# Performance work log

Hardware: AMD Instinct MI355X
Metric: run time of the kernel (lower is better)

Reference implementation:

```python
import jax, jax.numpy as jnp
import numpy as np
from jax import lax

U, K, POOL, STRIDE, FC = 300, 19, 7, 7, 100   # num_units, filter size, maxpool, fc_size
B, L, D = 256, 1000, 4                        # batch, seq len, DNA dim
P = (L - (K - 1) - (POOL - 1) - 1) // STRIDE + 1  # post_pool_size = 140
EPS = 1e-5  # BatchNorm eps (eval mode with running stats; Dropout is identity in eval)


def setup_inputs() -> dict:
    key = jax.random.key(0)
    ks = jax.random.split(key, 24)
    rn = lambda k, shp, s=0.1: jax.random.normal(k, shp, jnp.float32) * s
    return {
        "input_seq": jax.random.normal(ks[0], (B, L, D), jnp.float32),
        # per-unit conv (groups=U on tiled input == plain Conv1d(4, U, K))
        "w_conv": rn(ks[1], (U, D, K)), "b_conv": rn(ks[2], (U,)),
        "g1": 1.0 + rn(ks[3], (U,)), "be1": rn(ks[4], (U,)),
        "m1": rn(ks[5], (U,)), "v1": 1.0 + jax.random.uniform(ks[6], (U,), jnp.float32),
        # per-unit FC1 (grouped 1x1 conv: P -> FC per unit)
        "w_fc1": rn(ks[7], (U, FC, P)), "b_fc1": rn(ks[8], (U, FC)),
        "g2": 1.0 + rn(ks[9], (U, FC)), "be2": rn(ks[10], (U, FC)),
        "m2": rn(ks[11], (U, FC)), "v2": 1.0 + jax.random.uniform(ks[12], (U, FC), jnp.float32),
        # per-unit FC2 (grouped 1x1 conv: FC -> 1 per unit)
        "w_fc2": rn(ks[13], (U, FC)), "b_fc2": rn(ks[14], (U,)),
        "g3": 1.0 + rn(ks[15], (U,)), "be3": rn(ks[16], (U,)),
        "m3": rn(ks[17], (U,)), "v3": 1.0 + jax.random.uniform(ks[18], (U,), jnp.float32),
        # final Linear(U, 1)
        "w_out": rn(ks[19], (U, 1)), "b_out": rn(ks[20], (1,)),
    }


def reference(input_seq, w_conv, b_conv, g1, be1, m1, v1, w_fc1, b_fc1,
              g2, be2, m2, v2, w_fc2, b_fc2, g3, be3, m3, v3, w_out, b_out):
    x = jnp.transpose(input_seq, (0, 2, 1))  # B,D,L
    # grouped conv on input tiled U times: every group sees the same D=4 channels,
    # so it is exactly a plain Conv1d(D, U, K).
    conv = lax.conv_general_dilated(
        x, w_conv, (1,), 'VALID', dimension_numbers=('NCH', 'OIH', 'NCH')
    ) + b_conv[None, :, None]                 # B,U,L' (L'=L-K+1)
    a = (conv - m1[None, :, None]) * (g1 / jnp.sqrt(v1 + EPS))[None, :, None] + be1[None, :, None]
    a = jnp.exp(a)
    pooled = lax.reduce_window(a, -jnp.inf, lax.max,
                               (1, 1, POOL), (1, 1, STRIDE), 'VALID')  # B,U,P
    # Flatten->Unsqueeze->grouped 1x1 conv == per-unit matmul over P
    h = jnp.einsum('bup,ufp->buf', pooled, w_fc1) + b_fc1               # B,U,FC
    h = jax.nn.relu((h - m2) * (g2 / jnp.sqrt(v2 + EPS)) + be2)
    z = jnp.einsum('buf,uf->bu', h, w_fc2) + b_fc2                      # B,U
    z = jax.nn.relu((z - m3) * (g3 / jnp.sqrt(v3 + EPS)) + be3)
    return jax.nn.sigmoid(z @ w_out + b_out)                            # B,1
```

## Files before the change

kernel.cpp:

```cpp
#include <hip/hip_runtime.h>
#include <hip/hip_bf16.h>
#include <math.h>

#define U_   300
#define K_   19
#define FC_  100
#define B_   256
#define L_   1000
#define P_   140
#define EPS_ 1e-5f
#define WLD_ 144

typedef unsigned short ushort_t;
typedef __attribute__((ext_vector_type(8)))  short short8v;
typedef __attribute__((ext_vector_type(16))) float f32x16;

__device__ __forceinline__ ushort_t f2bf(float f) {
    union { float f; unsigned u; } a; a.f = f;
    unsigned r = a.u + 0x7fffu + ((a.u >> 16) & 1u);
    return (ushort_t)(r >> 16);
}

__global__ __launch_bounds__(256, 4)
void pack_conv_k(const float* __restrict__ w_conv, const float* __restrict__ b_conv,
                 const float* __restrict__ g1, const float* __restrict__ be1,
                 const float* __restrict__ m1, const float* __restrict__ v1,
                 ushort_t* __restrict__ w_bf, float* __restrict__ o1g)
{
    const int t = blockIdx.x * 256 + threadIdx.x;
    if (t < 320 * 80) {
        const int u = t / 80, j = t - u * 80;
        float val = 0.f;
        if (u < U_ && j < 76) {
            const int tp = j >> 2;
            const int d  = j & 3;
            const float s1 = g1[u] / sqrtf(v1[u] + EPS_);
            val = w_conv[u * 76 + 19 * d + tp] * s1;
        }
        const int nt = u >> 5, r = u & 31;
        const int kc = j >> 4, rem = j & 15;
        w_bf[nt * 2560 + kc * 512 + r * 16 + rem] = f2bf(val);
    }
    if (t < 320) {
        float o = 0.f;
        if (t < U_) {
            const float s1 = g1[t] / sqrtf(v1[t] + EPS_);
            o = (b_conv[t] - m1[t]) * s1 + be1[t];
        }
        o1g[t] = o;
    }
}

__global__ __launch_bounds__(896, 7)
void conv_mfma_k(const float4* __restrict__ x4,
                 const ushort_t* __restrict__ w_bf,
                 const float* __restrict__ o1g,
                 ushort_t* __restrict__ pooled)
{
    __shared__ ushort_t xls[880];
    const int tid = threadIdx.x;
    const int b   = blockIdx.y;
    const int bx  = blockIdx.x;
    const int w0  = bx * 28;
    const int l0  = w0 * 7;

    if (tid < 220) {
        const int gi = l0 + tid;
        float4 v = make_float4(0.f, 0.f, 0.f, 0.f);
        if (gi < L_) v = x4[(size_t)b * L_ + gi];
        ushort4 pk;
        pk.x = f2bf(v.x); pk.y = f2bf(v.y); pk.z = f2bf(v.z); pk.w = f2bf(v.w);
        *(ushort4*)&xls[4 * tid] = pk;
    }
    __syncthreads();

    const int lane = tid & 63;
    const int wv   = tid >> 6;
    const int mt   = (wv < 7) ? wv : wv - 7;
    const int nth  = (wv < 7) ? 0 : 1;
    const int half = lane >> 5;
    const int r32  = lane & 31;

    const int sreg = (r32 & 3) + 4 * (r32 >> 3);
    const int sh   = (r32 >> 2) & 1;
    const int off  = sreg < 7  ? sreg + 7 * sh
                   : sreg < 14 ? sreg + 7 + 7 * sh
                               : 28 + (sreg - 14) + 2 * sh;

    const char* xb = (const char*)xls + 8 * (28 * mt + off) + 16 * half;
    const char* wbase = (const char*)w_bf + 32 * r32 + 16 * half;

    short8v aA[5];
#pragma unroll
    for (int kc = 0; kc < 5; ++kc)
        aA[kc] = *(const short8v*)(xb + 32 * kc);

    const int pA = w0 + 4 * mt;
    const int nt0 = nth * 5;

    short8v bfr[5];
#pragma unroll
    for (int kc = 0; kc < 5; ++kc)
        bfr[kc] = *(const short8v*)(wbase + nt0 * 5120 + 1024 * kc);
    float o1u = o1g[nt0 * 32 + r32];

    for (int i = 0; i < 5; ++i) {
        const int nt  = nt0 + i;
        const int ntn = (i < 4) ? nt + 1 : nt;
        short8v bnx[5];
        const char* wn = wbase + ntn * 5120;
#pragma unroll
        for (int kc = 0; kc < 5; ++kc)
            bnx[kc] = *(const short8v*)(wn + 1024 * kc);
        const float o1n = o1g[ntn * 32 + r32];

        f32x16 acc = {};
#pragma unroll
        for (int kc = 0; kc < 5; ++kc)
            acc = __builtin_amdgcn_mfma_f32_32x32x16_bf16(aA[kc], bfr[kc], acc, 0, 0, 0);

        float m0 = acc[0], m1 = acc[7];
#pragma unroll
        for (int j = 1; j < 7; ++j)  m0 = fmaxf(m0, acc[j]);
#pragma unroll
        for (int j = 8; j < 14; ++j) m1 = fmaxf(m1, acc[j]);
        const unsigned pk = (unsigned)f2bf(__expf(m0 + o1u)) |
                            ((unsigned)f2bf(__expf(m1 + o1u)) << 16);
        const unsigned ot = __shfl_xor(pk, 32);

        const int u = nt * 32 + r32;
        if (u < U_ && half == 0) {
            ushort4 st;
            st.x = (ushort_t)(pk & 0xffff);
            st.y = (ushort_t)(ot & 0xffff);
            st.z = (ushort_t)(pk >> 16);
            st.w = (ushort_t)(ot >> 16);
            *(ushort4*)&pooled[((size_t)u * B_ + b) * P_ + pA] = st;
        }

#pragma unroll
        for (int kc = 0; kc < 5; ++kc) bfr[kc] = bnx[kc];
        o1u = o1n;
    }
}

__global__ __launch_bounds__(256, 3)
void fc_mfma_k(const ushort_t* __restrict__ pooled,
               const float* __restrict__ w_fc1,
               const float* __restrict__ b_fc1,
               const float* __restrict__ g2,
               const float* __restrict__ be2,
               const float* __restrict__ m2,
               const float* __restrict__ v2,
               const float* __restrict__ w_fc2,
               const float* __restrict__ b_fc2,
               const float* __restrict__ g3,
               const float* __restrict__ be3,
               const float* __restrict__ m3,
               const float* __restrict__ v3,
               float* __restrict__ zT)
{
    __shared__ ushort_t wlds[FC_ * WLD_];
    __shared__ float zred[128][33];
    const int tid  = threadIdx.x;
    const int u    = blockIdx.y;
    const int bt   = blockIdx.x;

    const float* __restrict__ wsrc = w_fc1 + (size_t)u * FC_ * P_;
    for (int idx = tid; idx < FC_ * 35; idx += 256) {
        const int f = idx / 35, j = idx - f * 35;
        const float4 v = *(const float4*)(wsrc + f * P_ + 4 * j);
        ushort4 pk;
        pk.x = f2bf(v.x); pk.y = f2bf(v.y); pk.z = f2bf(v.z); pk.w = f2bf(v.w);
        *(ushort4*)&wlds[f * WLD_ + 4 * j] = pk;
    }
    for (int idx = tid; idx < FC_ * 4; idx += 256) {
        const int f = idx >> 2, k = 140 + (idx & 3);
        wlds[f * WLD_ + k] = 0;
    }
    __syncthreads();

    const int lane = tid & 63;
    const int wv   = tid >> 6;
    const int half = lane >> 5;
    const int r32  = lane & 31;

    const int brow = bt * 128 + wv * 32 + r32;
    const ushort_t* __restrict__ abase =
        pooled + ((size_t)u * B_ + brow) * P_ + half * 8;

    const ushort_t* __restrict__ bl0 = &wlds[r32 * WLD_ + half * 8];
    const ushort_t* __restrict__ bl1 = &wlds[(32 + r32) * WLD_ + half * 8];
    const ushort_t* __restrict__ bl2 = &wlds[(64 + r32) * WLD_ + half * 8];
    const int f3c = (96 + r32 < FC_) ? (96 + r32) : (FC_ - 1);
    const ushort_t* __restrict__ bl3 = &wlds[f3c * WLD_ + half * 8];

    short8v ac = *(const short8v*)(abase);
    f32x16 acc0 = {}, acc1 = {}, acc2 = {}, acc3 = {};
#pragma unroll
    for (int kc = 0; kc < 9; ++kc) {
        const int kn = (kc < 8) ? kc + 1 : kc;
        const short8v an = *(const short8v*)(abase + kn * 16);
        const short8v b0 = *(const short8v*)(bl0 + kc * 16);
        const short8v b1 = *(const short8v*)(bl1 + kc * 16);
        const short8v b2 = *(const short8v*)(bl2 + kc * 16);
        const short8v b3 = *(const short8v*)(bl3 + kc * 16);
        acc0 = __builtin_amdgcn_mfma_f32_32x32x16_bf16(ac, b0, acc0, 0, 0, 0);
        acc1 = __builtin_amdgcn_mfma_f32_32x32x16_bf16(ac, b1, acc1, 0, 0, 0);
        acc2 = __builtin_amdgcn_mfma_f32_32x32x16_bf16(ac, b2, acc2, 0, 0, 0);
        acc3 = __builtin_amdgcn_mfma_f32_32x32x16_bf16(ac, b3, acc3, 0, 0, 0);
        ac = an;
    }

    float s2[4], o2[4], w2[4];
#pragma unroll
    for (int n = 0; n < 4; ++n) {
        const int f = n * 32 + r32;
        if (f < FC_) {
            const int fg = u * FC_ + f;
            const float ss = g2[fg] / sqrtf(v2[fg] + EPS_);
            s2[n] = ss;
            o2[n] = (b_fc1[fg] - m2[fg]) * ss + be2[fg];
            w2[n] = w_fc2[fg];
        } else {
            s2[n] = 0.f; o2[n] = 0.f; w2[n] = 0.f;
        }
    }
#pragma unroll
    for (int rg = 0; rg < 16; ++rg) {
        const int row = (rg & 3) + 8 * (rg >> 2) + 4 * half;
        float s = fmaxf(fmaf(acc0[rg], s2[0], o2[0]), 0.f) * w2[0];
        s = fmaf(fmaxf(fmaf(acc1[rg], s2[1], o2[1]), 0.f), w2[1], s);
        s = fmaf(fmaxf(fmaf(acc2[rg], s2[2], o2[2]), 0.f), w2[2], s);
        s = fmaf(fmaxf(fmaf(acc3[rg], s2[3], o2[3]), 0.f), w2[3], s);
        zred[wv * 32 + row][r32] = s;
    }
    __syncthreads();

    if (tid < 128) {
        float s = 0.f;
#pragma unroll
        for (int j = 0; j < 32; ++j) s += zred[tid][j];
        const float s3 = g3[u] / sqrtf(v3[u] + EPS_);
        const float o3 = (b_fc2[u] - m3[u]) * s3 + be3[u];
        zT[(size_t)(bt * 128 + tid) * 304 + u] = fmaxf(fmaf(s, s3, o3), 0.f);
    }
}

__global__ __launch_bounds__(64, 8)
void out_k(const float* __restrict__ zT,
           const float* __restrict__ w_out,
           const float* __restrict__ b_out,
           float* __restrict__ out)
{
    const int lane = threadIdx.x;
    const int b    = blockIdx.x;
    const float4* zr = (const float4*)(zT + (size_t)b * 304);
    const float4* w4 = (const float4*)w_out;

    float s = 0.f;
    for (int i = lane; i < 75; i += 64) {
        const float4 z = zr[i], w = w4[i];
        s += z.x * w.x + z.y * w.y + z.z * w.z + z.w * w.w;
    }
#pragma unroll
    for (int o = 32; o > 0; o >>= 1) s += __shfl_xor(s, o);
    if (lane == 0)
        out[b] = 1.0f / (1.0f + __expf(-(s + b_out[0])));
}

extern "C" void kernel_launch(void* const* d_in, const int* in_sizes, int n_in,
                              void* d_out, int out_size, void* d_ws, size_t ws_size,
                              hipStream_t stream)
{
    const float* input_seq = (const float*)d_in[0];
    const float* w_conv    = (const float*)d_in[1];
    const float* b_conv    = (const float*)d_in[2];
    const float* g1        = (const float*)d_in[3];
    const float* be1       = (const float*)d_in[4];
    const float* m1        = (const float*)d_in[5];
    const float* v1        = (const float*)d_in[6];
    const float* w_fc1     = (const float*)d_in[7];
    const float* b_fc1     = (const float*)d_in[8];
    const float* g2        = (const float*)d_in[9];
    const float* be2       = (const float*)d_in[10];
    const float* m2        = (const float*)d_in[11];
    const float* v2        = (const float*)d_in[12];
    const float* w_fc2     = (const float*)d_in[13];
    const float* b_fc2     = (const float*)d_in[14];
    const float* g3        = (const float*)d_in[15];
    const float* be3       = (const float*)d_in[16];
    const float* m3        = (const float*)d_in[17];
    const float* v3        = (const float*)d_in[18];
    const float* w_out     = (const float*)d_in[19];
    const float* b_out     = (const float*)d_in[20];

    char* p = (char*)d_ws;
    ushort_t* pooled = (ushort_t*)p;   p += (size_t)B_ * U_ * P_ * 2;
    ushort_t* w_bf   = (ushort_t*)p;   p += 320 * 80 * 2;
    float*    o1g    = (float*)p;      p += 320 * 4;
    float*    zT     = (float*)p;      p += (size_t)B_ * 304 * 4;

    pack_conv_k<<<dim3(100), 256, 0, stream>>>(
        w_conv, b_conv, g1, be1, m1, v1, w_bf, o1g);

    conv_mfma_k<<<dim3(5, B_), 896, 0, stream>>>(
        (const float4*)input_seq, w_bf, o1g, pooled);

    fc_mfma_k<<<dim3(2, U_), 256, 0, stream>>>(
        pooled, w_fc1, b_fc1, g2, be2, m2, v2, w_fc2, b_fc2,
        g3, be3, m3, v3, zT);

    out_k<<<dim3(B_), 64, 0, stream>>>(zT, w_out, b_out, (float*)d_out);
}
```

Measured before the change: 63.06 us.

## Process two batch rows per conv block and remap block ids for XCD locality

Each conv block now handles two batch samples with 7 waves, and every wave covers all 10 unit tiles. Each loaded weight fragment therefore feeds two MFMA chains, halving weight reloads per output and doubling independent MFMA work per wave. The software prefetch of the next weight tile is dropped. Both conv and FC grids become 1D with a swizzled block-id mapping, likely to group related blocks on the same XCD/L2 (the modulo-8 pattern suggests this) and improve cache reuse.

```diff
diff --git a/kernel.cpp b/kernel.cpp
--- a/kernel.cpp
+++ b/kernel.cpp
@@ -51,33 +51,36 @@
     }
 }
 
-__global__ __launch_bounds__(896, 7)
+__global__ __launch_bounds__(448, 4)
 void conv_mfma_k(const float4* __restrict__ x4,
                  const ushort_t* __restrict__ w_bf,
                  const float* __restrict__ o1g,
                  ushort_t* __restrict__ pooled)
 {
-    __shared__ ushort_t xls[880];
+    __shared__ ushort_t xls[2][880];
     const int tid = threadIdx.x;
-    const int b   = blockIdx.y;
-    const int bx  = blockIdx.x;
-    const int w0  = bx * 28;
-    const int l0  = w0 * 7;
-
-    if (tid < 220) {
-        const int gi = l0 + tid;
+    const int bid = blockIdx.x;
+    const int r8 = bid & 7, kk = bid >> 3;
+    const int bx = kk % 5, p8 = kk / 5;
+    const int pair = p8 * 8 + r8;
+    const int b0 = 2 * pair;
+    const int w0 = bx * 28;
+    const int l0 = w0 * 7;
+
+    if (tid < 440) {
+        const int which = (tid >= 220) ? 1 : 0;
+        const int i = tid - 220 * which;
+        const int gi = l0 + i;
         float4 v = make_float4(0.f, 0.f, 0.f, 0.f);
-        if (gi < L_) v = x4[(size_t)b * L_ + gi];
-        ushort4 pk;
-        pk.x = f2bf(v.x); pk.y = f2bf(v.y); pk.z = f2bf(v.z); pk.w = f2bf(v.w);
-        *(ushort4*)&xls[4 * tid] = pk;
+        if (gi < L_) v = x4[(size_t)(b0 + which) * L_ + gi];
+        ushort4 pk4;
+        pk4.x = f2bf(v.x); pk4.y = f2bf(v.y); pk4.z = f2bf(v.z); pk4.w = f2bf(v.w);
+        *(ushort4*)&xls[which][4 * i] = pk4;
     }
     __syncthreads();
 
     const int lane = tid & 63;
-    const int wv   = tid >> 6;
-    const int mt   = (wv < 7) ? wv : wv - 7;
-    const int nth  = (wv < 7) ? 0 : 1;
+    const int mt   = tid >> 6;
     const int half = lane >> 5;
     const int r32  = lane & 31;
 
@@ -87,60 +90,64 @@
                    : sreg < 14 ? sreg + 7 + 7 * sh
                                : 28 + (sreg - 14) + 2 * sh;
 
-    const char* xb = (const char*)xls + 8 * (28 * mt + off) + 16 * half;
+    const char* xb0 = (const char*)&xls[0][0] + 8 * (28 * mt + off) + 16 * half;
+    const char* xb1 = xb0 + 1760;
     const char* wbase = (const char*)w_bf + 32 * r32 + 16 * half;
 
-    short8v aA[5];
-#pragma unroll
-    for (int kc = 0; kc < 5; ++kc)
-        aA[kc] = *(const short8v*)(xb + 32 * kc);
+    short8v aA0[5], aA1[5];
+#pragma unroll
+    for (int kc = 0; kc < 5; ++kc) {
+        aA0[kc] = *(const short8v*)(xb0 + 32 * kc);
+        aA1[kc] = *(const short8v*)(xb1 + 32 * kc);
+    }
 
     const int pA = w0 + 4 * mt;
-    const int nt0 = nth * 5;
-
-    short8v bfr[5];
-#pragma unroll
-    for (int kc = 0; kc < 5; ++kc)
-        bfr[kc] = *(const short8v*)(wbase + nt0 * 5120 + 1024 * kc);
-    float o1u = o1g[nt0 * 32 + r32];
-
-    for (int i = 0; i < 5; ++i) {
-        const int nt  = nt0 + i;
-        const int ntn = (i < 4) ? nt + 1 : nt;
-        short8v bnx[5];
-        const char* wn = wbase + ntn * 5120;
+
+    for (int nt = 0; nt < 10; ++nt) {
+        short8v bfr[5];
+        const char* wn = wbase + nt * 5120;
 #pragma unroll
         for (int kc = 0; kc < 5; ++kc)
-            bnx[kc] = *(const short8v*)(wn + 1024 * kc);
-        const float o1n = o1g[ntn * 32 + r32];
-
-        f32x16 acc = {};
-#pragma unroll
-        for (int kc = 0; kc < 5; ++kc)
-            acc = __builtin_amdgcn_mfma_f32_32x32x16_bf16(aA[kc], bfr[kc], acc, 0, 0, 0);
-
-        float m0 = acc[0], m1 = acc[7];
-#pragma unroll
-        for (int j = 1; j < 7; ++j)  m0 = fmaxf(m0, acc[j]);
-#pragma unroll
-        for (int j = 8; j < 14; ++j) m1 = fmaxf(m1, acc[j]);
-        const unsigned pk = (unsigned)f2bf(__expf(m0 + o1u)) |
-                            ((unsigned)f2bf(__expf(m1 + o1u)) << 16);
-        const unsigned ot = __shfl_xor(pk, 32);
+            bfr[kc] = *(const short8v*)(wn + 1024 * kc);
+        const float o1u = o1g[nt * 32 + r32];
+
+        f32x16 acc0 = {};
+        f32x16 acc1 = {};
+#pragma unroll
+        for (int kc = 0; kc < 5; ++kc) {
+            acc0 = __builtin_amdgcn_mfma_f32_32x32x16_bf16(aA0[kc], bfr[kc], acc0, 0, 0, 0);
+            acc1 = __builtin_amdgcn_mfma_f32_32x32x16_bf16(aA1[kc], bfr[kc], acc1, 0, 0, 0);
+        }
+
+        float m00 = acc0[0], m01 = acc0[7];
+        float m10 = acc1[0], m11 = acc1[7];
+#pragma unroll
+        for (int j = 1; j < 7; ++j)  { m00 = fmaxf(m00, acc0[j]); m10 = fmaxf(m10, acc1[j]); }
+#pragma unroll
+        for (int j = 8; j < 14; ++j) { m01 = fmaxf(m01, acc0[j]); m11 = fmaxf(m11, acc1[j]); }
+
+        const unsigned pk0 = (unsigned)f2bf(__expf(m00 + o1u)) |
+                             ((unsigned)f2bf(__expf(m01 + o1u)) << 16);
+        const unsigned pk1 = (unsigned)f2bf(__expf(m10 + o1u)) |
+                             ((unsigned)f2bf(__expf(m11 + o1u)) << 16);
+        const unsigned ot0 = __shfl_xor(pk0, 32);
+        const unsigned ot1 = __shfl_xor(pk1, 32);
 
         const int u = nt * 32 + r32;
         if (u < U_ && half == 0) {
-            ushort4 st;
-            st.x = (ushort_t)(pk & 0xffff);
-            st.y = (ushort_t)(ot & 0xffff);
-            st.z = (ushort_t)(pk >> 16);
-            st.w = (ushort_t)(ot >> 16);
-            *(ushort4*)&pooled[((size_t)u * B_ + b) * P_ + pA] = st;
-        }
-
-#pragma unroll
-        for (int kc = 0; kc < 5; ++kc) bfr[kc] = bnx[kc];
-        o1u = o1n;
+            ushort4 st0, st1;
+            st0.x = (ushort_t)(pk0 & 0xffff);
+            st0.y = (ushort_t)(ot0 & 0xffff);
+            st0.z = (ushort_t)(pk0 >> 16);
+            st0.w = (ushort_t)(ot0 >> 16);
+            st1.x = (ushort_t)(pk1 & 0xffff);
+            st1.y = (ushort_t)(ot1 & 0xffff);
+            st1.z = (ushort_t)(pk1 >> 16);
+            st1.w = (ushort_t)(ot1 >> 16);
+            ushort_t* row = &pooled[((size_t)u * B_ + b0) * P_ + pA];
+            *(ushort4*)row         = st0;
+            *(ushort4*)(row + P_)  = st1;
+        }
     }
 }
 
@@ -163,8 +170,17 @@
     __shared__ ushort_t wlds[FC_ * WLD_];
     __shared__ float zred[128][33];
     const int tid  = threadIdx.x;
-    const int u    = blockIdx.y;
-    const int bt   = blockIdx.x;
+    const int bid = blockIdx.x;
+    int u, bt;
+    if (bid < 592) {
+        const int r = bid & 7, k = bid >> 3;
+        bt = k & 1;
+        u  = (k >> 1) * 8 + r;
+    } else {
+        const int t = bid - 592;
+        u  = 296 + (t >> 1);
+        bt = t & 1;
+    }
 
     const float* __restrict__ wsrc = w_fc1 + (size_t)u * FC_ * P_;
     for (int idx = tid; idx < FC_ * 35; idx += 256) {
@@ -304,10 +320,10 @@
     pack_conv_k<<<dim3(100), 256, 0, stream>>>(
         w_conv, b_conv, g1, be1, m1, v1, w_bf, o1g);
 
-    conv_mfma_k<<<dim3(5, B_), 896, 0, stream>>>(
+    conv_mfma_k<<<dim3(640), 448, 0, stream>>>(
         (const float4*)input_seq, w_bf, o1g, pooled);
 
-    fc_mfma_k<<<dim3(2, U_), 256, 0, stream>>>(
+    fc_mfma_k<<<dim3(600), 256, 0, stream>>>(
         pooled, w_fc1, b_fc1, g2, be2, m2, v2, w_fc2, b_fc2,
         g3, be3, m3, v3, zT);
 
```

Measured after the change: 64.79 us. +2.8%, slower.
